# Performance work log

Hardware: AMD Instinct MI355X
Metric: run time of the kernel (lower is better)

## Reference

```python
import jax, jax.numpy as jnp
import numpy as np

H = 0.5
EPS = 1e-08


def setup_inputs() -> dict:
    key = jax.random.key(0)
    k1, k2, k3 = jax.random.split(key, 3)
    B, in_dim, n_rules, out_dim = 16384, 64, 128, 32
    X = jax.random.normal(k1, (B, in_dim), dtype=jnp.float32)
    centers = jax.random.normal(k2, (in_dim, n_rules), dtype=jnp.float32)
    sigmas = jnp.ones((in_dim, n_rules), dtype=jnp.float32)
    W = jax.random.normal(k3, (out_dim, (in_dim + 1) * n_rules), dtype=jnp.float32) * 0.02
    b = jnp.zeros((out_dim,), dtype=jnp.float32)
    return {"X": X, "centers": centers, "sigmas": sigmas, "W": W, "b": b}


def reference(X, centers, sigmas, W, b):
    # HTSK firing levels: mean-style scaled Gaussian log-memberships summed over in_dim
    scale = H / sigmas ** 2 + EPS                      # [in_dim, n_rules]
    diff = X[:, :, None] - centers[None, :, :]          # [B, in_dim, n_rules]
    logits = jnp.sum(-(diff ** 2) * scale, axis=1)      # [B, n_rules]
    frs = jax.nn.softmax(logits, axis=1)                # [B, n_rules]
    B = X.shape[0]
    # order=1 consequent input: rule-major outer product, then raw firing levels
    xr = (frs[:, :, None] * X[:, None, :]).reshape(B, -1)  # [B, n_rules*in_dim]
    Z = jnp.concatenate([xr, frs], axis=1)               # [B, n_rules*(in_dim+1)]
    output = Z @ W.T + b                                 # [B, out_dim]
    return output, frs
```

## Files before the change

kernel.cpp:

```cpp
#include <hip/hip_runtime.h>


#define H_CONST 0.5f
#define EPS_CONST 1e-8f
#define NROWS 16384
#define NRULES 128
#define WCOLS 8320

typedef _Float16 half8 __attribute__((ext_vector_type(8)));
typedef float floatx4 __attribute__((ext_vector_type(4)));

#define MFMA16(a, b, c) __builtin_amdgcn_mfma_f32_16x16x32_f16((a), (b), (c), 0, 0, 0)

#define WFRAG_OFF 0
#define W0FRAG_OFF 262144
#define BMAT_OFF   (262144 + 4096)
#define KVEC_BYTE_OFF 630784
#define WS_BYTES_NEEDED (630784 + 512)

__global__ __launch_bounds__(256) void prep_kernel(
    const float* __restrict__ centers, const float* __restrict__ sigmas,
    const float* __restrict__ W, _Float16* __restrict__ wsh, float* __restrict__ kvec)
{
    __shared__ float sBuf[32 * 68];
    const int t = threadIdx.x;
    const int b = blockIdx.x;

    if (b < 128) {
        const int r = b;
        {
            int o = t >> 3, seg = t & 7;
            const float* g = W + o * WCOLS + r * 64 + seg * 8;
            floatx4 a = *(const floatx4*)g;
            floatx4 c = *(const floatx4*)(g + 4);
            *(floatx4*)(sBuf + o * 68 + seg * 8) = a;
            *(floatx4*)(sBuf + o * 68 + seg * 8 + 4) = c;
        }
        __syncthreads();
        {
            int L = t & 63, nt = (t >> 6) & 1, s = t >> 7;
            int o = nt * 16 + (L & 15);
            int ib = s * 32 + ((L >> 4) & 3) * 8;
            floatx4 fa = *(const floatx4*)(sBuf + o * 68 + ib);
            floatx4 fb = *(const floatx4*)(sBuf + o * 68 + ib + 4);
            half8 h;
#pragma unroll
            for (int k = 0; k < 8; ++k) h[k] = (_Float16)((k < 4) ? fa[k & 3] : fb[k & 3]);
            *(half8*)(wsh + WFRAG_OFF + r * 2048 + t * 8) = h;
        }
    } else if (b < 136) {
        const int nt = b - 128;
        float* sS = sBuf;
        float* sC = sBuf + 1088;
        {
            int i = t >> 2, c0 = (t & 3) * 4;
            floatx4 sg4 = *(const floatx4*)(sigmas + i * NRULES + nt * 16 + c0);
            floatx4 ct4 = *(const floatx4*)(centers + i * NRULES + nt * 16 + c0);
#pragma unroll
            for (int k = 0; k < 4; ++k) { sS[i * 17 + c0 + k] = sg4[k]; sC[i * 17 + c0 + k] = ct4[k]; }
        }
        __syncthreads();
#pragma unroll
        for (int kk = 0; kk < 3; ++kk) {
            int unit = t + kk * 256;
            int s = unit >> 6, L = unit & 63;
            int q = (L >> 4) & 3, nl = L & 15;
            int g = s >> 1;
            int i0 = (s & 1) * 32 + q * 8;
            half8 h;
#pragma unroll
            for (int j = 0; j < 8; ++j) {
                int i = i0 + j;
                float sg = sS[i * 17 + nl];
                float S = H_CONST / (sg * sg) + EPS_CONST;
                float c = sC[i * 17 + nl];
                float CS2 = 2.0f * c * S;
                _Float16 v;
                if (g == 0 || g == 2) v = -(_Float16)S;
                else if (g == 1) { _Float16 sh = (_Float16)S; v = -(_Float16)(S - (float)sh); }
                else if (g == 3 || g == 5) v = (_Float16)CS2;
                else { _Float16 ch = (_Float16)CS2; v = (_Float16)(CS2 - (float)ch); }
                h[j] = v;
            }
            *(half8*)(wsh + BMAT_OFF + ((s * 8 + nt) * 64 + L) * 8) = h;
        }
    } else {
#pragma unroll
        for (int kk = 0; kk < 2; ++kk) {
            int unit = t + kk * 256;
            int s = unit >> 7, nt = (unit >> 6) & 1, L = unit & 63;
            int q = (L >> 4) & 3;
            int o = nt * 16 + (L & 15);
            half8 h;
#pragma unroll
            for (int j = 0; j < 8; ++j) {
                int r = s * 32 + q * 8 + j;
                h[j] = (_Float16)W[o * WCOLS + 8192 + r];
            }
            *(half8*)(wsh + W0FRAG_OFF + ((s * 2 + nt) * 64 + L) * 8) = h;
        }
        if (t < 128) {
            int r = t;
            float acc = 0.f;
#pragma unroll 8
            for (int i = 0; i < 64; ++i) {
                float sg = sigmas[i * NRULES + r];
                float S = H_CONST / (sg * sg) + EPS_CONST;
                float c = centers[i * NRULES + r];
                acc += c * c * S;
            }
            kvec[r] = acc;
        }
    }
}

__global__ __launch_bounds__(256) void main_fused(
    const float* __restrict__ X, const float* __restrict__ bias,
    const _Float16* __restrict__ wsh, const float* __restrict__ kvec,
    float* __restrict__ out, float* __restrict__ frs_out)
{
    __shared__ _Float16 sXh[32 * 64];
    __shared__ _Float16 sXl[32 * 64];
    __shared__ _Float16 sX2h[32 * 64];
    __shared__ _Float16 sX2l[32 * 64];
    __shared__ _Float16 sF[32 * 136];
    __shared__ float sU[4608];

    const int t = threadIdx.x;
    const int w = t >> 6;
    const int L = t & 63;
    const int m = L & 15;
    const int q = L >> 4;
    const int row0 = blockIdx.x * 32;

    const _Float16* Bm = wsh + BMAT_OFF;
    half8 Bv[12][2];
#pragma unroll
    for (int s = 0; s < 12; ++s) {
        Bv[s][0] = *(const half8*)(Bm + ((s * 8 + 2 * w + 0) * 64 + L) * 8);
        Bv[s][1] = *(const half8*)(Bm + ((s * 8 + 2 * w + 1) * 64 + L) * 8);
    }
    float kv0 = kvec[(2 * w + 0) * 16 + m];
    float kv1 = kvec[(2 * w + 1) * 16 + m];

    {
        int row = t >> 3, uc = t & 7;
        const float* gx = X + (row0 + row) * 64 + uc * 8;
        floatx4 xa = *(const floatx4*)gx;
        floatx4 xb = *(const floatx4*)(gx + 4);
        int base = row * 64 + (uc ^ (row & 7)) * 8;
        half8 vh, vl, v2h, v2l;
#pragma unroll
        for (int k = 0; k < 8; ++k) {
            float x = (k < 4) ? xa[k & 3] : xb[k & 3];
            _Float16 xh = (_Float16)x;
            _Float16 xl2 = (_Float16)(x - (float)xh);
            float x2 = x * x;
            _Float16 x2h = (_Float16)x2;
            _Float16 x2l = (_Float16)(x2 - (float)x2h);
            vh[k] = xh; vl[k] = xl2; v2h[k] = x2h; v2l[k] = x2l;
        }
        *(half8*)(sXh + base) = vh;
        *(half8*)(sXl + base) = vl;
        *(half8*)(sX2h + base) = v2h;
        *(half8*)(sX2l + base) = v2l;
    }
    __syncthreads();

    floatx4 lacc[2][2];
#pragma unroll
    for (int mt = 0; mt < 2; ++mt)
#pragma unroll
        for (int n = 0; n < 2; ++n) lacc[mt][n] = (floatx4){0.f, 0.f, 0.f, 0.f};

#pragma unroll
    for (int s = 0; s < 12; ++s) {
        const _Float16* arr = (s < 4) ? sX2h : (s < 6) ? sX2l : (s < 10) ? sXh : sXl;
        int phys = (((s & 1) << 2) | q) ^ (m & 7);
#pragma unroll
        for (int mt = 0; mt < 2; ++mt) {
            half8 a = *(const half8*)(arr + (mt * 16 + m) * 64 + phys * 8);
            lacc[mt][0] = MFMA16(a, Bv[s][0], lacc[mt][0]);
            lacc[mt][1] = MFMA16(a, Bv[s][1], lacc[mt][1]);
        }
    }

#pragma unroll
    for (int mt = 0; mt < 2; ++mt)
#pragma unroll
        for (int ntl = 0; ntl < 2; ++ntl)
#pragma unroll
            for (int reg = 0; reg < 4; ++reg) {
                int rl = mt * 16 + q * 4 + reg;
                int col = (2 * w + ntl) * 16 + m;
                sU[rl * 132 + col] = lacc[mt][ntl][reg] - (ntl ? kv1 : kv0);
            }

    const int rq = w;
    const int r0 = rq * 32;
    const _Float16* Wf = wsh + WFRAG_OFF;
    const _Float16* W0f = wsh + W0FRAG_OFF;
#define LDW(r, slot) (*(const half8*)(Wf + (r) * 2048 + ((slot) * 64 + L) * 8))

    half8 ring[4][4];
#pragma unroll
    for (int p = 0; p < 4; ++p) {
        ring[p][0] = LDW(r0 + p, 0);
        ring[p][1] = LDW(r0 + p, 1);
        ring[p][2] = LDW(r0 + p, 2);
        ring[p][3] = LDW(r0 + p, 3);
    }
    half8 wb0 = *(const half8*)(W0f + ((rq * 2 + 0) * 64 + L) * 8);
    half8 wb1 = *(const half8*)(W0f + ((rq * 2 + 1) * 64 + L) * 8);

    __syncthreads();

    {
        int row = t >> 3, l8 = t & 7;
        int base = row * 132 + l8 * 16;
        float v[16];
        float mx = -1e30f;
#pragma unroll
        for (int k = 0; k < 16; ++k) { v[k] = sU[base + k]; mx = fmaxf(mx, v[k]); }
        mx = fmaxf(mx, __shfl_xor(mx, 1));
        mx = fmaxf(mx, __shfl_xor(mx, 2));
        mx = fmaxf(mx, __shfl_xor(mx, 4));
        float sum = 0.f;
#pragma unroll
        for (int k = 0; k < 16; ++k) { v[k] = __expf(v[k] - mx); sum += v[k]; }
        sum += __shfl_xor(sum, 1);
        sum += __shfl_xor(sum, 2);
        sum += __shfl_xor(sum, 4);
        float inv = 1.0f / sum;
        float* gf = frs_out + (row0 + row) * 128 + l8 * 16;
        half8 h0, h1;
#pragma unroll
        for (int c = 0; c < 4; ++c) {
            floatx4 o4;
#pragma unroll
            for (int k = 0; k < 4; ++k) {
                float f = v[c * 4 + k] * inv;
                o4[k] = f;
                if (c < 2) h0[c * 4 + k] = (_Float16)f; else h1[(c - 2) * 4 + k] = (_Float16)f;
            }
            *(floatx4*)(gf + c * 4) = o4;
        }
        *(half8*)(sF + row * 136 + l8 * 16) = h0;
        *(half8*)(sF + row * 136 + l8 * 16 + 8) = h1;
    }
    __syncthreads();

    half8 xf[2][2];
#pragma unroll
    for (int mt = 0; mt < 2; ++mt)
#pragma unroll
        for (int s = 0; s < 2; ++s) {
            int phys = ((s << 2) | q) ^ (m & 7);
            xf[mt][s] = *(const half8*)(sXh + (mt * 16 + m) * 64 + phys * 8);
        }

    floatx4 oacc[2][2];
#pragma unroll
    for (int mt = 0; mt < 2; ++mt)
#pragma unroll
        for (int n = 0; n < 2; ++n) oacc[mt][n] = (floatx4){0.f, 0.f, 0.f, 0.f};

#pragma unroll
    for (int rg = 0; rg < 4; ++rg) {
        half8 fv0 = *(const half8*)(sF + (0 * 16 + m) * 136 + r0 + rg * 8);
        half8 fv1 = *(const half8*)(sF + (1 * 16 + m) * 136 + r0 + rg * 8);
#pragma unroll
        for (int rr2 = 0; rr2 < 8; ++rr2) {
            int rr = rg * 8 + rr2;
            int slot = rr & 3;
            half8 c00 = ring[slot][0], c01 = ring[slot][1];
            half8 c10 = ring[slot][2], c11 = ring[slot][3];
            if (rr < 28) {
                int rn = r0 + rr + 4;
                ring[slot][0] = LDW(rn, 0);
                ring[slot][1] = LDW(rn, 1);
                ring[slot][2] = LDW(rn, 2);
                ring[slot][3] = LDW(rn, 3);
            }
            _Float16 f0 = fv0[rr2], f1 = fv1[rr2];
            half8 fs0, fs1;
#pragma unroll
            for (int k = 0; k < 8; ++k) { fs0[k] = f0; fs1[k] = f1; }
            half8 a00 = fs0 * xf[0][0];
            half8 a01 = fs0 * xf[0][1];
            half8 a10 = fs1 * xf[1][0];
            half8 a11 = fs1 * xf[1][1];
            oacc[0][0] = MFMA16(a00, c00, oacc[0][0]);
            oacc[0][0] = MFMA16(a01, c10, oacc[0][0]);
            oacc[0][1] = MFMA16(a00, c01, oacc[0][1]);
            oacc[0][1] = MFMA16(a01, c11, oacc[0][1]);
            oacc[1][0] = MFMA16(a10, c00, oacc[1][0]);
            oacc[1][0] = MFMA16(a11, c10, oacc[1][0]);
            oacc[1][1] = MFMA16(a10, c01, oacc[1][1]);
            oacc[1][1] = MFMA16(a11, c11, oacc[1][1]);
        }
    }

    {
#pragma unroll
        for (int mt = 0; mt < 2; ++mt) {
            half8 a = *(const half8*)(sF + (mt * 16 + m) * 136 + rq * 32 + q * 8);
            oacc[mt][0] = MFMA16(a, wb0, oacc[mt][0]);
            oacc[mt][1] = MFMA16(a, wb1, oacc[mt][1]);
        }
    }

#pragma unroll
    for (int mt = 0; mt < 2; ++mt)
#pragma unroll
        for (int ntl = 0; ntl < 2; ++ntl)
#pragma unroll
            for (int reg = 0; reg < 4; ++reg)
                sU[w * 1152 + (mt * 16 + q * 4 + reg) * 36 + ntl * 16 + m] = oacc[mt][ntl][reg];
    __syncthreads();

    {
        int row = t >> 3, col0 = (t & 7) * 4;
        floatx4 acc = *(const floatx4*)(sU + 0 * 1152 + row * 36 + col0);
        acc += *(const floatx4*)(sU + 1 * 1152 + row * 36 + col0);
        acc += *(const floatx4*)(sU + 2 * 1152 + row * 36 + col0);
        acc += *(const floatx4*)(sU + 3 * 1152 + row * 36 + col0);
        acc += *(const floatx4*)(bias + col0);
        *(floatx4*)(out + (row0 + row) * 32 + col0) = acc;
    }
#undef LDW
}

extern "C" void kernel_launch(void* const* d_in, const int* in_sizes, int n_in,
                              void* d_out, int out_size, void* d_ws, size_t ws_size,
                              hipStream_t stream) {
    const float* X = (const float*)d_in[0];
    const float* centers = (const float*)d_in[1];
    const float* sigmas = (const float*)d_in[2];
    const float* W = (const float*)d_in[3];
    const float* b = (const float*)d_in[4];
    float* outp = (float*)d_out;
    float* frs_out = outp + NROWS * 32;
    if (ws_size < (size_t)WS_BYTES_NEEDED) return;
    _Float16* wsh = (_Float16*)d_ws;
    float* kvec = (float*)((char*)d_ws + KVEC_BYTE_OFF);

    prep_kernel<<<137, 256, 0, stream>>>(centers, sigmas, W, wsh, kvec);
    main_fused<<<NROWS / 32, 256, 0, stream>>>(X, b, wsh, kvec, outp, frs_out);
}
```

Measured before the change: 84.81 us.

## Deepen W prefetch ring, hoist global loads, defer firing-level stores

Several scheduling changes go into the fused kernel. The X and W0 fragment loads are issued at kernel start. The W fragment prefetch ring grows from 4 to 8 rules deep. All firing-level fragments are preloaded from LDS before the MFMA loop. The fp32 frs output store moves to the end of the kernel, where it is rebuilt from the fp16 copy in LDS. A min-blocks-per-SM hint of 2 is added to launch_bounds. The goal is more latency hiding for global loads and less store traffic in the critical section. In exchange, register pressure rises, with a risk of spills under the occupancy hint, and frs is now written with fp16 precision.

```diff
diff --git a/kernel.cpp b/kernel.cpp
--- a/kernel.cpp
+++ b/kernel.cpp
@@ -114,7 +114,7 @@
     }
 }
 
-__global__ __launch_bounds__(256) void main_fused(
+__global__ __launch_bounds__(256, 2) void main_fused(
     const float* __restrict__ X, const float* __restrict__ bias,
     const _Float16* __restrict__ wsh, const float* __restrict__ kvec,
     float* __restrict__ out, float* __restrict__ frs_out)
@@ -133,6 +133,11 @@
     const int q = L >> 4;
     const int row0 = blockIdx.x * 32;
 
+    const int arow = t >> 3, auc = t & 7;
+    const float* gx = X + (row0 + arow) * 64 + auc * 8;
+    floatx4 xa = *(const floatx4*)gx;
+    floatx4 xb = *(const floatx4*)(gx + 4);
+
     const _Float16* Bm = wsh + BMAT_OFF;
     half8 Bv[12][2];
 #pragma unroll
@@ -143,12 +148,16 @@
     float kv0 = kvec[(2 * w + 0) * 16 + m];
     float kv1 = kvec[(2 * w + 1) * 16 + m];
 
-    {
-        int row = t >> 3, uc = t & 7;
-        const float* gx = X + (row0 + row) * 64 + uc * 8;
-        floatx4 xa = *(const floatx4*)gx;
-        floatx4 xb = *(const floatx4*)(gx + 4);
-        int base = row * 64 + (uc ^ (row & 7)) * 8;
+    const int rq = w;
+    const int r0 = rq * 32;
+    const _Float16* Wf = wsh + WFRAG_OFF;
+    const _Float16* W0f = wsh + W0FRAG_OFF;
+#define LDW(r, slot) (*(const half8*)(Wf + (r) * 2048 + ((slot) * 64 + L) * 8))
+    half8 wb0 = *(const half8*)(W0f + ((rq * 2 + 0) * 64 + L) * 8);
+    half8 wb1 = *(const half8*)(W0f + ((rq * 2 + 1) * 64 + L) * 8);
+
+    {
+        int base = arow * 64 + (auc ^ (arow & 7)) * 8;
         half8 vh, vl, v2h, v2l;
 #pragma unroll
         for (int k = 0; k < 8; ++k) {
@@ -196,22 +205,14 @@
                 sU[rl * 132 + col] = lacc[mt][ntl][reg] - (ntl ? kv1 : kv0);
             }
 
-    const int rq = w;
-    const int r0 = rq * 32;
-    const _Float16* Wf = wsh + WFRAG_OFF;
-    const _Float16* W0f = wsh + W0FRAG_OFF;
-#define LDW(r, slot) (*(const half8*)(Wf + (r) * 2048 + ((slot) * 64 + L) * 8))
-
-    half8 ring[4][4];
-#pragma unroll
-    for (int p = 0; p < 4; ++p) {
+    half8 ring[8][4];
+#pragma unroll
+    for (int p = 0; p < 8; ++p) {
         ring[p][0] = LDW(r0 + p, 0);
         ring[p][1] = LDW(r0 + p, 1);
         ring[p][2] = LDW(r0 + p, 2);
         ring[p][3] = LDW(r0 + p, 3);
     }
-    half8 wb0 = *(const half8*)(W0f + ((rq * 2 + 0) * 64 + L) * 8);
-    half8 wb1 = *(const half8*)(W0f + ((rq * 2 + 1) * 64 + L) * 8);
 
     __syncthreads();
 
@@ -232,18 +233,11 @@
         sum += __shfl_xor(sum, 2);
         sum += __shfl_xor(sum, 4);
         float inv = 1.0f / sum;
-        float* gf = frs_out + (row0 + row) * 128 + l8 * 16;
         half8 h0, h1;
 #pragma unroll
-        for (int c = 0; c < 4; ++c) {
-            floatx4 o4;
-#pragma unroll
-            for (int k = 0; k < 4; ++k) {
-                float f = v[c * 4 + k] * inv;
-                o4[k] = f;
-                if (c < 2) h0[c * 4 + k] = (_Float16)f; else h1[(c - 2) * 4 + k] = (_Float16)f;
-            }
-            *(floatx4*)(gf + c * 4) = o4;
+        for (int k = 0; k < 8; ++k) {
+            h0[k] = (_Float16)(v[k] * inv);
+            h1[k] = (_Float16)(v[k + 8] * inv);
         }
         *(half8*)(sF + row * 136 + l8 * 16) = h0;
         *(half8*)(sF + row * 136 + l8 * 16 + 8) = h1;
@@ -259,6 +253,13 @@
             xf[mt][s] = *(const half8*)(sXh + (mt * 16 + m) * 64 + phys * 8);
         }
 
+    half8 fvA[4], fvB[4];
+#pragma unroll
+    for (int rg = 0; rg < 4; ++rg) {
+        fvA[rg] = *(const half8*)(sF + (0 * 16 + m) * 136 + r0 + rg * 8);
+        fvB[rg] = *(const half8*)(sF + (1 * 16 + m) * 136 + r0 + rg * 8);
+    }
+
     floatx4 oacc[2][2];
 #pragma unroll
     for (int mt = 0; mt < 2; ++mt)
@@ -267,22 +268,20 @@
 
 #pragma unroll
     for (int rg = 0; rg < 4; ++rg) {
-        half8 fv0 = *(const half8*)(sF + (0 * 16 + m) * 136 + r0 + rg * 8);
-        half8 fv1 = *(const half8*)(sF + (1 * 16 + m) * 136 + r0 + rg * 8);
 #pragma unroll
         for (int rr2 = 0; rr2 < 8; ++rr2) {
             int rr = rg * 8 + rr2;
-            int slot = rr & 3;
+            int slot = rr & 7;
             half8 c00 = ring[slot][0], c01 = ring[slot][1];
             half8 c10 = ring[slot][2], c11 = ring[slot][3];
-            if (rr < 28) {
-                int rn = r0 + rr + 4;
+            if (rr < 24) {
+                int rn = r0 + rr + 8;
                 ring[slot][0] = LDW(rn, 0);
                 ring[slot][1] = LDW(rn, 1);
                 ring[slot][2] = LDW(rn, 2);
                 ring[slot][3] = LDW(rn, 3);
             }
-            _Float16 f0 = fv0[rr2], f1 = fv1[rr2];
+            _Float16 f0 = fvA[rg][rr2], f1 = fvB[rg][rr2];
             half8 fs0, fs1;
 #pragma unroll
             for (int k = 0; k < 8; ++k) { fs0[k] = f0; fs1[k] = f1; }
@@ -328,6 +327,24 @@
         acc += *(const floatx4*)(bias + col0);
         *(floatx4*)(out + (row0 + row) * 32 + col0) = acc;
     }
+    {
+        int row = t >> 3, l8 = t & 7;
+        half8 h0 = *(const half8*)(sF + row * 136 + l8 * 16);
+        half8 h1 = *(const half8*)(sF + row * 136 + l8 * 16 + 8);
+        float* gf = frs_out + (row0 + row) * 128 + l8 * 16;
+        floatx4 f0, f1, f2, f3;
+#pragma unroll
+        for (int k = 0; k < 4; ++k) {
+            f0[k] = (float)h0[k];
+            f1[k] = (float)h0[k + 4];
+            f2[k] = (float)h1[k];
+            f3[k] = (float)h1[k + 4];
+        }
+        *(floatx4*)gf = f0;
+        *(floatx4*)(gf + 4) = f1;
+        *(floatx4*)(gf + 8) = f2;
+        *(floatx4*)(gf + 12) = f3;
+    }
 #undef LDW
 }
 
```

Result: no change. 86.10 us (+1.5%).

## Process 64 rows per block to reuse W fragments across more M-tiles

Applied to the files above, without the earlier changes.

Doubles the row tile from 32 to 64 per workgroup, so each wave runs 4 M-tiles instead of 2 against the same streamed W fragments and B matrix registers. This halves the global W traffic per row and halves the grid size to 256 blocks. In exchange it uses twice the LDS and more accumulator registers, which may lower occupancy. With only 256 blocks, the grid may also underfill the GPU's compute units.

```diff
diff --git a/kernel.cpp b/kernel.cpp
--- a/kernel.cpp
+++ b/kernel.cpp
@@ -119,19 +119,19 @@
     const _Float16* __restrict__ wsh, const float* __restrict__ kvec,
     float* __restrict__ out, float* __restrict__ frs_out)
 {
-    __shared__ _Float16 sXh[32 * 64];
-    __shared__ _Float16 sXl[32 * 64];
-    __shared__ _Float16 sX2h[32 * 64];
-    __shared__ _Float16 sX2l[32 * 64];
-    __shared__ _Float16 sF[32 * 136];
-    __shared__ float sU[4608];
+    __shared__ _Float16 sXh[64 * 64];
+    __shared__ _Float16 sXl[64 * 64];
+    __shared__ _Float16 sX2h[64 * 64];
+    __shared__ _Float16 sX2l[64 * 64];
+    __shared__ _Float16 sF[64 * 136];
+    __shared__ float sU[9216];
 
     const int t = threadIdx.x;
     const int w = t >> 6;
     const int L = t & 63;
     const int m = L & 15;
     const int q = L >> 4;
-    const int row0 = blockIdx.x * 32;
+    const int row0 = blockIdx.x * 64;
 
     const _Float16* Bm = wsh + BMAT_OFF;
     half8 Bv[12][2];
@@ -143,8 +143,10 @@
     float kv0 = kvec[(2 * w + 0) * 16 + m];
     float kv1 = kvec[(2 * w + 1) * 16 + m];
 
-    {
-        int row = t >> 3, uc = t & 7;
+#pragma unroll
+    for (int uu = 0; uu < 2; ++uu) {
+        int u = t + uu * 256;
+        int row = u >> 3, uc = u & 7;
         const float* gx = X + (row0 + row) * 64 + uc * 8;
         floatx4 xa = *(const floatx4*)gx;
         floatx4 xb = *(const floatx4*)(gx + 4);
@@ -167,9 +169,9 @@
     }
     __syncthreads();
 
-    floatx4 lacc[2][2];
-#pragma unroll
-    for (int mt = 0; mt < 2; ++mt)
+    floatx4 lacc[4][2];
+#pragma unroll
+    for (int mt = 0; mt < 4; ++mt)
 #pragma unroll
         for (int n = 0; n < 2; ++n) lacc[mt][n] = (floatx4){0.f, 0.f, 0.f, 0.f};
 
@@ -178,7 +180,7 @@
         const _Float16* arr = (s < 4) ? sX2h : (s < 6) ? sX2l : (s < 10) ? sXh : sXl;
         int phys = (((s & 1) << 2) | q) ^ (m & 7);
 #pragma unroll
-        for (int mt = 0; mt < 2; ++mt) {
+        for (int mt = 0; mt < 4; ++mt) {
             half8 a = *(const half8*)(arr + (mt * 16 + m) * 64 + phys * 8);
             lacc[mt][0] = MFMA16(a, Bv[s][0], lacc[mt][0]);
             lacc[mt][1] = MFMA16(a, Bv[s][1], lacc[mt][1]);
@@ -186,7 +188,7 @@
     }
 
 #pragma unroll
-    for (int mt = 0; mt < 2; ++mt)
+    for (int mt = 0; mt < 4; ++mt)
 #pragma unroll
         for (int ntl = 0; ntl < 2; ++ntl)
 #pragma unroll
@@ -215,8 +217,9 @@
 
     __syncthreads();
 
-    {
-        int row = t >> 3, l8 = t & 7;
+#pragma unroll
+    for (int h = 0; h < 2; ++h) {
+        int row = h * 32 + (t >> 3), l8 = t & 7;
         int base = row * 132 + l8 * 16;
         float v[16];
         float mx = -1e30f;
@@ -250,31 +253,34 @@
     }
     __syncthreads();
 
-    half8 xf[2][2];
-#pragma unroll
-    for (int mt = 0; mt < 2; ++mt)
+    half8 xf[4][2];
+#pragma unroll
+    for (int mt = 0; mt < 4; ++mt)
 #pragma unroll
         for (int s = 0; s < 2; ++s) {
             int phys = ((s << 2) | q) ^ (m & 7);
             xf[mt][s] = *(const half8*)(sXh + (mt * 16 + m) * 64 + phys * 8);
         }
 
-    floatx4 oacc[2][2];
-#pragma unroll
-    for (int mt = 0; mt < 2; ++mt)
+    floatx4 oacc[4][2];
+#pragma unroll
+    for (int mt = 0; mt < 4; ++mt)
 #pragma unroll
         for (int n = 0; n < 2; ++n) oacc[mt][n] = (floatx4){0.f, 0.f, 0.f, 0.f};
 
 #pragma unroll
     for (int rg = 0; rg < 4; ++rg) {
-        half8 fv0 = *(const half8*)(sF + (0 * 16 + m) * 136 + r0 + rg * 8);
-        half8 fv1 = *(const half8*)(sF + (1 * 16 + m) * 136 + r0 + rg * 8);
+        half8 fvm[4];
+#pragma unroll
+        for (int mt = 0; mt < 4; ++mt)
+            fvm[mt] = *(const half8*)(sF + (mt * 16 + m) * 136 + r0 + rg * 8);
 #pragma unroll
         for (int rr2 = 0; rr2 < 8; ++rr2) {
             int rr = rg * 8 + rr2;
             int slot = rr & 3;
-            half8 c00 = ring[slot][0], c01 = ring[slot][1];
-            half8 c10 = ring[slot][2], c11 = ring[slot][3];
+            half8 cw[2][2];
+            cw[0][0] = ring[slot][0]; cw[0][1] = ring[slot][1];
+            cw[1][0] = ring[slot][2]; cw[1][1] = ring[slot][3];
             if (rr < 28) {
                 int rn = r0 + rr + 4;
                 ring[slot][0] = LDW(rn, 0);
@@ -282,51 +288,54 @@
                 ring[slot][2] = LDW(rn, 2);
                 ring[slot][3] = LDW(rn, 3);
             }
-            _Float16 f0 = fv0[rr2], f1 = fv1[rr2];
-            half8 fs0, fs1;
-#pragma unroll
-            for (int k = 0; k < 8; ++k) { fs0[k] = f0; fs1[k] = f1; }
-            half8 a00 = fs0 * xf[0][0];
-            half8 a01 = fs0 * xf[0][1];
-            half8 a10 = fs1 * xf[1][0];
-            half8 a11 = fs1 * xf[1][1];
-            oacc[0][0] = MFMA16(a00, c00, oacc[0][0]);
-            oacc[0][0] = MFMA16(a01, c10, oacc[0][0]);
-            oacc[0][1] = MFMA16(a00, c01, oacc[0][1]);
-            oacc[0][1] = MFMA16(a01, c11, oacc[0][1]);
-            oacc[1][0] = MFMA16(a10, c00, oacc[1][0]);
-            oacc[1][0] = MFMA16(a11, c10, oacc[1][0]);
-            oacc[1][1] = MFMA16(a10, c01, oacc[1][1]);
-            oacc[1][1] = MFMA16(a11, c11, oacc[1][1]);
-        }
-    }
+            half8 am[4][2];
+#pragma unroll
+            for (int mt = 0; mt < 4; ++mt) {
+                _Float16 f = fvm[mt][rr2];
+                half8 fs;
+#pragma unroll
+                for (int k = 0; k < 8; ++k) fs[k] = f;
+                am[mt][0] = fs * xf[mt][0];
+                am[mt][1] = fs * xf[mt][1];
+            }
+#pragma unroll
+            for (int s = 0; s < 2; ++s)
+#pragma unroll
+                for (int nt = 0; nt < 2; ++nt)
+#pragma unroll
+                    for (int mt = 0; mt < 4; ++mt)
+                        oacc[mt][nt] = MFMA16(am[mt][s], cw[s][nt], oacc[mt][nt]);
+        }
+    }
+
+#pragma unroll
+    for (int mt = 0; mt < 4; ++mt) {
+        half8 a = *(const half8*)(sF + (mt * 16 + m) * 136 + rq * 32 + q * 8);
+        oacc[mt][0] = MFMA16(a, wb0, oacc[mt][0]);
+        oacc[mt][1] = MFMA16(a, wb1, oacc[mt][1]);
+    }
+
+#pragma unroll
+    for (int mt = 0; mt < 4; ++mt)
+#pragma unroll
+        for (int ntl = 0; ntl < 2; ++ntl)
+#pragma unroll
+            for (int reg = 0; reg < 4; ++reg)
+                sU[w * 2304 + (mt * 16 + q * 4 + reg) * 36 + ntl * 16 + m] = oacc[mt][ntl][reg];
+    __syncthreads();
 
     {
-#pragma unroll
-        for (int mt = 0; mt < 2; ++mt) {
-            half8 a = *(const half8*)(sF + (mt * 16 + m) * 136 + rq * 32 + q * 8);
-            oacc[mt][0] = MFMA16(a, wb0, oacc[mt][0]);
-            oacc[mt][1] = MFMA16(a, wb1, oacc[mt][1]);
-        }
-    }
-
-#pragma unroll
-    for (int mt = 0; mt < 2; ++mt)
-#pragma unroll
-        for (int ntl = 0; ntl < 2; ++ntl)
-#pragma unroll
-            for (int reg = 0; reg < 4; ++reg)
-                sU[w * 1152 + (mt * 16 + q * 4 + reg) * 36 + ntl * 16 + m] = oacc[mt][ntl][reg];
-    __syncthreads();
-
-    {
-        int row = t >> 3, col0 = (t & 7) * 4;
-        floatx4 acc = *(const floatx4*)(sU + 0 * 1152 + row * 36 + col0);
-        acc += *(const floatx4*)(sU + 1 * 1152 + row * 36 + col0);
-        acc += *(const floatx4*)(sU + 2 * 1152 + row * 36 + col0);
-        acc += *(const floatx4*)(sU + 3 * 1152 + row * 36 + col0);
-        acc += *(const floatx4*)(bias + col0);
-        *(floatx4*)(out + (row0 + row) * 32 + col0) = acc;
+        int row = t >> 2, col0 = (t & 3) * 8;
+#pragma unroll
+        for (int hh = 0; hh < 2; ++hh) {
+            int col = col0 + hh * 4;
+            floatx4 acc = *(const floatx4*)(sU + 0 * 2304 + row * 36 + col);
+            acc += *(const floatx4*)(sU + 1 * 2304 + row * 36 + col);
+            acc += *(const floatx4*)(sU + 2 * 2304 + row * 36 + col);
+            acc += *(const floatx4*)(sU + 3 * 2304 + row * 36 + col);
+            acc += *(const floatx4*)(bias + col);
+            *(floatx4*)(out + (row0 + row) * 32 + col) = acc;
+        }
     }
 #undef LDW
 }
@@ -346,5 +355,5 @@
     float* kvec = (float*)((char*)d_ws + KVEC_BYTE_OFF);
 
     prep_kernel<<<137, 256, 0, stream>>>(centers, sigmas, W, wsh, kvec);
-    main_fused<<<NROWS / 32, 256, 0, stream>>>(X, b, wsh, kvec, outp, frs_out);
+    main_fused<<<NROWS / 64, 256, 0, stream>>>(X, b, wsh, kvec, outp, frs_out);
 }
```

After: 90.21 us. 6.4% more time.
